# Optimization experiments

Measured on AMD Instinct MI355X. Metric: run time of the kernel, lower is better.

Reference implementation:

```python
import jax, jax.numpy as jnp
import numpy as np

B, N, D, K = 32, 196, 1024, 512  # batch, tokens (14x14), feature dim, prototypes
EPS = 1e-8  # torch F.cosine_similarity default eps


def setup_inputs() -> dict:
    key = jax.random.key(0)
    ks = jax.random.split(key, 8)
    z = jax.random.normal(ks[0], (B, N, D), jnp.float32)
    prototypes = jax.random.normal(ks[1], (K, D), jnp.float32)  # nn.Parameter(randn)
    gate_w = jax.random.normal(ks[2], (2 * D, D), jnp.float32) * 0.02  # Linear(2D->D), stored [in,out]
    gate_b = jnp.zeros((D,), jnp.float32)
    dec_w = jax.random.normal(ks[3], (D, 7 * 7 * 512), jnp.float32) * 0.02
    dec_b = jnp.zeros((7 * 7 * 512,), jnp.float32)
    ct1_w = jax.random.normal(ks[4], (512, 256, 4, 4), jnp.float32) * 0.02  # torch [in,out,kh,kw]
    ct1_b = jnp.zeros((256,), jnp.float32)
    ct2_w = jax.random.normal(ks[5], (256, 3, 4, 4), jnp.float32) * 0.02
    ct2_b = jnp.zeros((3,), jnp.float32)
    return dict(z=z, prototypes=prototypes, gate_w=gate_w, gate_b=gate_b,
                dec_w=dec_w, dec_b=dec_b, ct1_w=ct1_w, ct1_b=ct1_b,
                ct2_w=ct2_w, ct2_b=ct2_b)


def _conv_transpose(x, w, b):
    # ConvTranspose2d(k=4, stride=2, pad=1) == conv with lhs_dilation=2,
    # padding k-1-pad=2, spatially-flipped kernel, torch weight layout [in,out,kh,kw] -> IOHW.
    wf = jnp.flip(w, (2, 3))
    y = jax.lax.conv_general_dilated(
        x, wf, window_strides=(1, 1), padding=((2, 2), (2, 2)),
        lhs_dilation=(2, 2), dimension_numbers=("NCHW", "IOHW", "NCHW"))
    return y + b[None, :, None, None]


def reference(z, prototypes, gate_w, gate_b, dec_w, dec_b, ct1_w, ct1_b, ct2_w, ct2_b):
    # MemoryBank: cosine similarity of every token against every prototype
    zn = jnp.linalg.norm(z, axis=-1, keepdims=True)            # [B,N,1]
    pn = jnp.linalg.norm(prototypes, axis=-1)                  # [K]
    dots = jnp.einsum('bnd,kd->bnk', z, prototypes)            # [B,N,K]
    sim = dots / jnp.maximum(zn * pn[None, None, :], EPS)
    attn = jax.nn.softmax(sim, axis=-1)                        # [B,N,K]
    z_hat = jnp.einsum('bnk,kd->bnd', attn, prototypes)        # [B,N,D]
    # GatedFusion: sigmoid gate over concat(z, z_hat)
    gate = jax.nn.sigmoid(jnp.concatenate([z, z_hat], axis=-1) @ gate_w + gate_b)
    z_fused = gate * z + (1.0 - gate) * z_hat                  # [B,N,D]
    # Decoder (original reshape is shape-inconsistent; pool tokens -> [B,D])
    pooled = z_fused.mean(axis=1)                              # [B,D]
    h = (pooled @ dec_w + dec_b).reshape(-1, 512, 7, 7)
    h = jax.nn.relu(_conv_transpose(h, ct1_w, ct1_b))          # [B,256,14,14]
    x_recon = _conv_transpose(h, ct2_w, ct2_b)                 # [B,3,28,28]
    return x_recon, attn
```

## Files before the change

### kernel.cpp

```cpp
#include <hip/hip_runtime.h>
#include <cstdint>
#include <cstddef>
#include <cmath>

#define EPS_COS 1e-8f

typedef unsigned short u16;
typedef __attribute__((ext_vector_type(8))) short short8v;
typedef __attribute__((ext_vector_type(4))) short short4v;
typedef __attribute__((ext_vector_type(4))) float f32x4;

__device__ __forceinline__ u16 f2bf(float x) {
    unsigned int u = __float_as_uint(x);
    return (u16)((u + 0x7FFFu + ((u >> 16) & 1u)) >> 16);
}
__device__ __forceinline__ float bf2f(u16 h) {
    return __uint_as_float(((unsigned int)h) << 16);
}

__global__ __launch_bounds__(256) void norm_cvt_kernel(const float* __restrict__ src,
                                                       u16* __restrict__ dst, int dstStride,
                                                       float* __restrict__ norms) {
    int r = blockIdx.x;
    int t = threadIdx.x;
    const float4 v = *reinterpret_cast<const float4*>(&src[(size_t)r * 1024 + t * 4]);
    short4v o;
    o[0] = f2bf(v.x); o[1] = f2bf(v.y); o[2] = f2bf(v.z); o[3] = f2bf(v.w);
    *reinterpret_cast<short4v*>(&dst[(size_t)r * dstStride + t * 4]) = o;
    float ss = v.x * v.x + v.y * v.y + v.z * v.z + v.w * v.w;
#pragma unroll
    for (int off = 32; off > 0; off >>= 1) ss += __shfl_down(ss, off);
    __shared__ float red[4];
    int wave = t >> 6, lane = t & 63;
    if (lane == 0) red[wave] = ss;
    __syncthreads();
    if (t == 0) norms[r] = sqrtf(red[0] + red[1] + red[2] + red[3]);
}

__global__ __launch_bounds__(256) void transpose_cvt_kernel(const float* __restrict__ src,
                                                            u16* __restrict__ dst,
                                                            int R, int C) {
    __shared__ float tile[64][65];
    int c0 = blockIdx.x * 64, r0 = blockIdx.y * 64;
    int t = threadIdx.x;
#pragma unroll
    for (int j = 0; j < 16; ++j) {
        int idx = j * 256 + t;
        int r = idx >> 6, c = idx & 63;
        tile[r][c] = src[(size_t)(r0 + r) * C + c0 + c];
    }
    __syncthreads();
#pragma unroll
    for (int j = 0; j < 16; ++j) {
        int idx = j * 256 + t;
        int c = idx >> 6, r = idx & 63;
        dst[(size_t)(c0 + c) * R + r0 + r] = f2bf(tile[r][c]);
    }
}

__global__ __launch_bounds__(256) void prep_kernel(u16* __restrict__ hp,
                                                   const float* __restrict__ ct1w,
                                                   u16* __restrict__ wt,
                                                   const float* __restrict__ ct2w,
                                                   u16* __restrict__ wpad,
                                                   float* __restrict__ pooled) {
    int idx = blockIdx.x * 256 + threadIdx.x;
    if (idx < 165888) {
        short8v zv = {0, 0, 0, 0, 0, 0, 0, 0};
        *reinterpret_cast<short8v*>(hp + (size_t)idx * 8) = zv;
    } else if (idx < 165888 + 131072) {
        int i = idx - 165888;
        int oc = i & 255, ic = i >> 8;
        float v[16];
#pragma unroll
        for (int j = 0; j < 16; ++j) v[j] = ct1w[(size_t)i * 16 + j];
#pragma unroll
        for (int pp = 0; pp < 4; ++pp) {
            int py = pp >> 1, px = pp & 1;
#pragma unroll
            for (int tap = 0; tap < 4; ++tap) {
                int ty = tap >> 1, tx = tap & 1;
                int ky = (1 - py) + 2 * ty;
                int kx = (1 - px) + 2 * tx;
                wt[((size_t)(pp * 256 + oc)) * 2048 + ic * 4 + tap] = f2bf(v[ky * 4 + kx]);
            }
        }
    } else if (idx < 165888 + 131072 + 16384) {
        int i = idx - 165888 - 131072;
        int ic = i & 255;
        int col = i >> 8;
        float v = 0.0f;
        if (col < 48) {
            int kx = col & 3, ky = (col >> 2) & 3, oc = col >> 4;
            v = ct2w[((size_t)ic * 3 + oc) * 16 + ky * 4 + kx];
        }
        wpad[i] = f2bf(v);
    } else {
        int i = idx - 165888 - 131072 - 16384;
        *reinterpret_cast<f32x4*>(pooled + (size_t)i * 4) = (f32x4){0.f, 0.f, 0.f, 0.f};
    }
}

template <int FM, int FN, int EPI>
__global__ __launch_bounds__(256) void mfma_gemm_kernel(
    const u16* __restrict__ A, int sA, size_t zsA,
    const u16* __restrict__ B, int sB, size_t zsB,
    int M, int N, int K,
    float* __restrict__ Cf,
    u16* __restrict__ Cb, int sCb,
    const float* __restrict__ bias,
    const float* __restrict__ zf32,
    const u16* __restrict__ zhbf, int szh,
    float* __restrict__ outf) {
    constexpr int BM = FM * 32, BN = FN * 32;
    constexpr int NA = (BM * 4) / 256;
    constexpr int NB = (BN * 4) / 256;
    __shared__ __align__(16) u16 As[BM * 32];
    __shared__ __align__(16) u16 Bs[BN * 32];
    A += (size_t)blockIdx.z * zsA;
    B += (size_t)blockIdx.z * zsB;
    const int t = threadIdx.x;
    const int lane = t & 63;
    const int wid = t >> 6;
    const int wm = wid >> 1, wn = wid & 1;
    const int m0 = blockIdx.x * BM, n0 = blockIdx.y * BN;
    const int g = lane >> 4, lr = lane & 15;

    f32x4 acc[FM][FN];
#pragma unroll
    for (int i = 0; i < FM; ++i)
#pragma unroll
        for (int j = 0; j < FN; ++j) acc[i][j] = (f32x4){0.f, 0.f, 0.f, 0.f};

    short8v ra[NA], rb[NB];
#pragma unroll
    for (int j = 0; j < NA; ++j) {
        int c = j * 256 + t, row = c >> 2, ck = (c & 3) ^ ((row >> 1) & 3);
        ra[j] = *reinterpret_cast<const short8v*>(A + (size_t)(m0 + row) * sA + ck * 8);
    }
#pragma unroll
    for (int j = 0; j < NB; ++j) {
        int c = j * 256 + t, row = c >> 2, ck = (c & 3) ^ ((row >> 1) & 3);
        rb[j] = *reinterpret_cast<const short8v*>(B + (size_t)(n0 + row) * sB + ck * 8);
    }

    for (int k0 = 0; k0 < K; k0 += 32) {
        __syncthreads();
#pragma unroll
        for (int j = 0; j < NA; ++j)
            *reinterpret_cast<short8v*>(As + ((j * 256 + t) << 3)) = ra[j];
#pragma unroll
        for (int j = 0; j < NB; ++j)
            *reinterpret_cast<short8v*>(Bs + ((j * 256 + t) << 3)) = rb[j];
        __syncthreads();
        if (k0 + 32 < K) {
#pragma unroll
            for (int j = 0; j < NA; ++j) {
                int c = j * 256 + t, row = c >> 2, ck = (c & 3) ^ ((row >> 1) & 3);
                ra[j] = *reinterpret_cast<const short8v*>(A + (size_t)(m0 + row) * sA + k0 + 32 + ck * 8);
            }
#pragma unroll
            for (int j = 0; j < NB; ++j) {
                int c = j * 256 + t, row = c >> 2, ck = (c & 3) ^ ((row >> 1) & 3);
                rb[j] = *reinterpret_cast<const short8v*>(B + (size_t)(n0 + row) * sB + k0 + 32 + ck * 8);
            }
        }
        short8v af[FM], bfr[FN];
#pragma unroll
        for (int fm = 0; fm < FM; ++fm) {
            int row = wm * (FM * 16) + fm * 16 + lr;
            int ck = g ^ ((row >> 1) & 3);
            af[fm] = *reinterpret_cast<const short8v*>(As + row * 32 + ck * 8);
        }
#pragma unroll
        for (int fn = 0; fn < FN; ++fn) {
            int col = wn * (FN * 16) + fn * 16 + lr;
            int ck = g ^ ((col >> 1) & 3);
            bfr[fn] = *reinterpret_cast<const short8v*>(Bs + col * 32 + ck * 8);
        }
#pragma unroll
        for (int fm = 0; fm < FM; ++fm)
#pragma unroll
            for (int fn = 0; fn < FN; ++fn)
                acc[fm][fn] = __builtin_amdgcn_mfma_f32_16x16x32_bf16(
                    af[fm], bfr[fn], acc[fm][fn], 0, 0, 0);
    }

    if (EPI == 2) {
#pragma unroll
        for (int fn = 0; fn < FN; ++fn) {
            int col = n0 + wn * (FN * 16) + fn * 16 + lr;
            int base = m0 + wm * (FM * 16) + g * 4;
            int b0 = base / 196;
            float p0 = 0.f, p1 = 0.f;
#pragma unroll
            for (int fm = 0; fm < FM; ++fm) {
#pragma unroll
                for (int r = 0; r < 4; ++r) {
                    int row = base + fm * 16 + r;
                    float v = acc[fm][fn][r];
                    float gs = 1.0f / (1.0f + __expf(-(v + bias[col])));
                    float zv = zf32[(size_t)row * N + col];
                    float zh = bf2f(zhbf[(size_t)row * szh + col]);
                    float fused = gs * zv + (1.0f - gs) * zh;
                    bool same = (row / 196) == b0;
                    p0 += same ? fused : 0.f;
                    p1 += same ? 0.f : fused;
                }
            }
            atomicAdd(&outf[(size_t)b0 * 1024 + col], p0);
            if (p1 != 0.f) atomicAdd(&outf[(size_t)(b0 + 1) * 1024 + col], p1);
        }
    } else {
#pragma unroll
        for (int fm = 0; fm < FM; ++fm) {
#pragma unroll
            for (int fn = 0; fn < FN; ++fn) {
#pragma unroll
                for (int r = 0; r < 4; ++r) {
                    int row = m0 + wm * (FM * 16) + fm * 16 + g * 4 + r;
                    int col = n0 + wn * (FN * 16) + fn * 16 + lr;
                    float v = acc[fm][fn][r];
                    if (EPI == 0) {
                        Cf[(size_t)row * N + col] = v;
                    } else if (EPI == 1) {
                        Cb[(size_t)row * sCb + col] = f2bf(v);
                    } else {
                        if (row < 1568) {
                            float vv = fmaxf(v + bias[col], 0.0f);
                            int bb = row / 49, ss = row - bb * 49;
                            Cb[(((size_t)bb * 4 + blockIdx.z) * 49 + ss) * 256 + col] = f2bf(vv);
                        }
                    }
                }
            }
        }
    }
}

__global__ __launch_bounds__(256) void softmax_kernel(const float* __restrict__ dots,
                                                      const float* __restrict__ zn,
                                                      const float* __restrict__ pn,
                                                      float* __restrict__ attn,
                                                      u16* __restrict__ attn_bf) {
    int m = blockIdx.x;
    int t = threadIdx.x;
    float zm = zn[m];
    float d0 = dots[(size_t)m * 512 + t];
    float d1 = dots[(size_t)m * 512 + t + 256];
    float v0 = d0 / fmaxf(zm * pn[t], EPS_COS);
    float v1 = d1 / fmaxf(zm * pn[t + 256], EPS_COS);
    float mx = fmaxf(v0, v1);
#pragma unroll
    for (int off = 32; off > 0; off >>= 1) mx = fmaxf(mx, __shfl_down(mx, off));
    __shared__ float red[8];
    int wave = t >> 6, lane = t & 63;
    if (lane == 0) red[wave] = mx;
    __syncthreads();
    if (t == 0) red[4] = fmaxf(fmaxf(red[0], red[1]), fmaxf(red[2], red[3]));
    __syncthreads();
    mx = red[4];
    float e0 = expf(v0 - mx), e1 = expf(v1 - mx);
    float s = e0 + e1;
#pragma unroll
    for (int off = 32; off > 0; off >>= 1) s += __shfl_down(s, off);
    if (lane == 0) red[wave] = s;
    __syncthreads();
    if (t == 0) red[5] = 1.0f / (red[0] + red[1] + red[2] + red[3]);
    __syncthreads();
    float r = red[5];
    float a0 = e0 * r, a1 = e1 * r;
    attn[(size_t)m * 512 + t] = a0;
    attn[(size_t)m * 512 + t + 256] = a1;
    attn_bf[(size_t)m * 512 + t] = f2bf(a0);
    attn_bf[(size_t)m * 512 + t + 256] = f2bf(a1);
}

#define DEC_KC 128
__global__ __launch_bounds__(256) void dec_split_kernel(const float* __restrict__ pooled,
                                                        const float* __restrict__ dec_w,
                                                        float* __restrict__ partial) {
    const int t = threadIdx.x;
    const int lane = t & 63;
    const int wv = t >> 6;
    const int c = blockIdx.x * 256 + lane * 4;
    const int kc = blockIdx.y;
    __shared__ float pl[32][DEC_KC];
    for (int i = t; i < 32 * DEC_KC; i += 256) {
        int b = i >> 7, kk = i & (DEC_KC - 1);
        pl[b][kk] = pooled[(size_t)b * 1024 + kc * DEC_KC + kk] * (1.0f / 196.0f);
    }
    __syncthreads();
    f32x4 acc[8];
#pragma unroll
    for (int j = 0; j < 8; ++j) acc[j] = (f32x4){0.f, 0.f, 0.f, 0.f};
    const float* wp = dec_w + (size_t)(kc * DEC_KC) * 25088 + c;
#pragma unroll 8
    for (int k = 0; k < DEC_KC; ++k) {
        f32x4 w4 = *reinterpret_cast<const f32x4*>(wp + (size_t)k * 25088);
#pragma unroll
        for (int j = 0; j < 8; ++j) {
            float pv = pl[wv * 8 + j][k];
            acc[j].x = fmaf(pv, w4.x, acc[j].x);
            acc[j].y = fmaf(pv, w4.y, acc[j].y);
            acc[j].z = fmaf(pv, w4.z, acc[j].z);
            acc[j].w = fmaf(pv, w4.w, acc[j].w);
        }
    }
#pragma unroll
    for (int j = 0; j < 8; ++j) {
        int b = wv * 8 + j;
        *reinterpret_cast<f32x4*>(partial + ((size_t)kc * 32 + b) * 25088 + c) = acc[j];
    }
}

__global__ __launch_bounds__(256) void dec_reduce_kernel(const float* __restrict__ partial,
                                                         const float* __restrict__ dec_b,
                                                         u16* __restrict__ hp) {
    int c = blockIdx.x * 256 + threadIdx.x;
    int b = blockIdx.y;
    float s = dec_b[c];
#pragma unroll
    for (int kc = 0; kc < 8; ++kc)
        s += partial[((size_t)kc * 32 + b) * 25088 + c];
    int ic = c / 49, sp = c - ic * 49;
    int sy = sp / 7, sx = sp - sy * 7;
    hp[((size_t)b * 512 + ic) * 81 + (sy + 1) * 9 + sx + 1] = f2bf(s);
}

__global__ __launch_bounds__(256) void im2col_kernel(const u16* __restrict__ hp,
                                                     u16* __restrict__ A) {
    int idx = blockIdx.x * 256 + threadIdx.x;
    int k8 = idx & 255;
    int pr = idx >> 8;
    int p = pr / 1600;
    int row = pr - p * 1600;
    short8v o = {0, 0, 0, 0, 0, 0, 0, 0};
    if (row < 1568) {
        int b = row / 49, s = row - b * 49;
        int sy = s / 7, sx = s - sy * 7;
        int r0 = sy + (p >> 1) + 1;
        int c0 = sx + (p & 1) + 1;
        int ic0 = k8 * 2;
        const u16* hb = hp + ((size_t)b * 512 + ic0) * 81;
#pragma unroll
        for (int j = 0; j < 2; ++j) {
            o[j * 4 + 0] = hb[r0 * 9 + c0];
            o[j * 4 + 1] = hb[r0 * 9 + c0 - 1];
            o[j * 4 + 2] = hb[(r0 - 1) * 9 + c0];
            o[j * 4 + 3] = hb[(r0 - 1) * 9 + c0 - 1];
            hb += 81;
        }
    }
    *reinterpret_cast<short8v*>(A + (size_t)idx * 8) = o;
}

__global__ __launch_bounds__(256) void convt2_gather_kernel(const float* __restrict__ G,
                                                            const float* __restrict__ bias,
                                                            float* __restrict__ out) {
    int o = blockIdx.x * 256 + threadIdx.x;
    int ox = o % 28;
    int oy = (o / 28) % 28;
    int oc = (o / 784) % 3;
    int b = o / 2352;
    int by = (oy + 1) >> 1, bx = (ox + 1) >> 1;
    float acc = bias[oc];
#pragma unroll
    for (int ty = 0; ty < 2; ++ty) {
        int iy = by - ty;
        if ((unsigned)iy >= 14u) continue;
#pragma unroll
        for (int tx = 0; tx < 2; ++tx) {
            int ix = bx - tx;
            if ((unsigned)ix >= 14u) continue;
            int p = (iy & 1) * 2 + (ix & 1);
            int row = ((b * 4 + p) * 49) + (iy >> 1) * 7 + (ix >> 1);
            int ky = oy + 1 - 2 * iy, kx = ox + 1 - 2 * ix;
            acc += G[(size_t)row * 64 + oc * 16 + ky * 4 + kx];
        }
    }
    out[o] = acc;
}

extern "C" void kernel_launch(void* const* d_in, const int* in_sizes, int n_in,
                              void* d_out, int out_size, void* d_ws, size_t ws_size,
                              hipStream_t stream) {
    const float* z      = (const float*)d_in[0];
    const float* protos = (const float*)d_in[1];
    const float* gate_w = (const float*)d_in[2];
    const float* gate_b = (const float*)d_in[3];
    const float* dec_w  = (const float*)d_in[4];
    const float* dec_b  = (const float*)d_in[5];
    const float* ct1_w  = (const float*)d_in[6];
    const float* ct1_b  = (const float*)d_in[7];
    const float* ct2_w  = (const float*)d_in[8];
    const float* ct2_b  = (const float*)d_in[9];

    float* xout = (float*)d_out;
    float* attn = xout + 75264;

    float* w = (float*)d_ws;
    float* pn        = w;
    float* zn        = w + 512;
    float* pooled    = w + 6784;
    u16*   wt1bf     = (u16*)(w + 51840);
    u16*   protos_bf = (u16*)(w + 1100416);
    u16*   protosT   = (u16*)(w + 1362560);
    u16*   gwT       = (u16*)(w + 1624704);
    u16*   attn_bf   = (u16*)(w + 2673280);
    u16*   Abig      = (u16*)(w + 4278912);
    u16*   A_cls     = (u16*)(w + 2673280);
    float* dots      = w + 10701440;
    float* partial   = w + 10701440;
    u16*   h2cb      = (u16*)(w + 11364992);
    u16*   hp        = (u16*)(w + 17123968);
    float* G         = w + 17787520;
    u16*   wpad      = (u16*)(w + 18188928);

    prep_kernel<<<1256, 256, 0, stream>>>(hp, ct1_w, wt1bf, ct2_w, wpad, pooled);
    norm_cvt_kernel<<<6272, 256, 0, stream>>>(z, Abig, 2048, zn);
    norm_cvt_kernel<<<512, 256, 0, stream>>>(protos, protos_bf, 1024, pn);
    transpose_cvt_kernel<<<dim3(16, 8), 256, 0, stream>>>(protos, protosT, 512, 1024);
    transpose_cvt_kernel<<<dim3(16, 32), 256, 0, stream>>>(gate_w, gwT, 2048, 1024);
    mfma_gemm_kernel<2, 4, 0><<<dim3(98, 4), 256, 0, stream>>>(
        Abig, 2048, 0, protos_bf, 1024, 0, 6272, 512, 1024,
        dots, nullptr, 0, nullptr, nullptr, nullptr, 0, nullptr);
    softmax_kernel<<<6272, 256, 0, stream>>>(dots, zn, pn, attn, attn_bf);
    mfma_gemm_kernel<4, 4, 1><<<dim3(49, 8), 256, 0, stream>>>(
        attn_bf, 512, 0, protosT, 512, 0, 6272, 1024, 512,
        nullptr, Abig + 1024, 2048, nullptr, nullptr, nullptr, 0, nullptr);
    mfma_gemm_kernel<4, 4, 2><<<dim3(49, 8), 256, 0, stream>>>(
        Abig, 2048, 0, gwT, 2048, 0, 6272, 1024, 2048,
        nullptr, nullptr, 0, gate_b, z, Abig + 1024, 2048, pooled);
    dec_split_kernel<<<dim3(98, 8), 256, 0, stream>>>(pooled, dec_w, partial);
    dec_reduce_kernel<<<dim3(98, 32), 256, 0, stream>>>(partial, dec_b, hp);
    im2col_kernel<<<6400, 256, 0, stream>>>(hp, A_cls);
    mfma_gemm_kernel<2, 2, 3><<<dim3(25, 4, 4), 256, 0, stream>>>(
        A_cls, 2048, (size_t)1600 * 2048, wt1bf, 2048, (size_t)256 * 2048,
        1600, 256, 2048, nullptr, h2cb, 0, ct1_b, nullptr, nullptr, 0, nullptr);
    mfma_gemm_kernel<2, 2, 0><<<dim3(98, 1), 256, 0, stream>>>(
        h2cb, 256, 0, wpad, 256, 0, 6272, 64, 256,
        G, nullptr, 0, nullptr, nullptr, nullptr, 0, nullptr);
    convt2_gather_kernel<<<294, 256, 0, stream>>>(G, ct2_b, xout);
}
```

Measured before the change: 220.5 us.

## Widen GEMM K-tile to 64, add block swizzle, bf16 z epilogue, pipeline decoder loads

The MFMA GEMM now stages 64-wide K tiles with an XOR bank swizzle, so there are half as many barrier round-trips per K. An optional grid remap groups blocks (intended for XCD/L2 locality) and is enabled on the three large GEMMs. The gated-fusion epilogue reads z from the bf16 copy instead of fp32, which halves that traffic but adds rounding error to the pooled result. The decoder split kernel software-pipelines its weight loads four rows ahead to hide global latency.

```diff
diff --git a/kernel.cpp b/kernel.cpp
--- a/kernel.cpp
+++ b/kernel.cpp
@@ -101,7 +101,7 @@
     }
 }
 
-template <int FM, int FN, int EPI>
+template <int FM, int FN, int EPI, bool SWZ>
 __global__ __launch_bounds__(256) void mfma_gemm_kernel(
     const u16* __restrict__ A, int sA, size_t zsA,
     const u16* __restrict__ B, int sB, size_t zsB,
@@ -109,21 +109,30 @@
     float* __restrict__ Cf,
     u16* __restrict__ Cb, int sCb,
     const float* __restrict__ bias,
-    const float* __restrict__ zf32,
+    const u16* __restrict__ zbf,
     const u16* __restrict__ zhbf, int szh,
     float* __restrict__ outf) {
     constexpr int BM = FM * 32, BN = FN * 32;
-    constexpr int NA = (BM * 4) / 256;
-    constexpr int NB = (BN * 4) / 256;
-    __shared__ __align__(16) u16 As[BM * 32];
-    __shared__ __align__(16) u16 Bs[BN * 32];
+    constexpr int NA = BM / 32;
+    constexpr int NB = BN / 32;
+    __shared__ __align__(16) u16 As[BM * 64];
+    __shared__ __align__(16) u16 Bs[BN * 64];
+    int bx = blockIdx.x, by = blockIdx.y;
+    if (SWZ) {
+        int gx = gridDim.x;
+        int nwg = gx * gridDim.y;
+        int lb = by * gx + bx;
+        int flat = (lb & 7) * (nwg >> 3) + (lb >> 3);
+        bx = flat % gx;
+        by = flat / gx;
+    }
     A += (size_t)blockIdx.z * zsA;
     B += (size_t)blockIdx.z * zsB;
     const int t = threadIdx.x;
     const int lane = t & 63;
     const int wid = t >> 6;
     const int wm = wid >> 1, wn = wid & 1;
-    const int m0 = blockIdx.x * BM, n0 = blockIdx.y * BN;
+    const int m0 = bx * BM, n0 = by * BN;
     const int g = lane >> 4, lr = lane & 15;
 
     f32x4 acc[FM][FN];
@@ -135,55 +144,62 @@
     short8v ra[NA], rb[NB];
 #pragma unroll
     for (int j = 0; j < NA; ++j) {
-        int c = j * 256 + t, row = c >> 2, ck = (c & 3) ^ ((row >> 1) & 3);
+        int c = j * 256 + t, row = c >> 3, ck = c & 7;
         ra[j] = *reinterpret_cast<const short8v*>(A + (size_t)(m0 + row) * sA + ck * 8);
     }
 #pragma unroll
     for (int j = 0; j < NB; ++j) {
-        int c = j * 256 + t, row = c >> 2, ck = (c & 3) ^ ((row >> 1) & 3);
+        int c = j * 256 + t, row = c >> 3, ck = c & 7;
         rb[j] = *reinterpret_cast<const short8v*>(B + (size_t)(n0 + row) * sB + ck * 8);
     }
 
-    for (int k0 = 0; k0 < K; k0 += 32) {
+    for (int k0 = 0; k0 < K; k0 += 64) {
         __syncthreads();
 #pragma unroll
-        for (int j = 0; j < NA; ++j)
-            *reinterpret_cast<short8v*>(As + ((j * 256 + t) << 3)) = ra[j];
-#pragma unroll
-        for (int j = 0; j < NB; ++j)
-            *reinterpret_cast<short8v*>(Bs + ((j * 256 + t) << 3)) = rb[j];
+        for (int j = 0; j < NA; ++j) {
+            int c = j * 256 + t, row = c >> 3, ck = c & 7;
+            *reinterpret_cast<short8v*>(As + row * 64 + ((ck ^ (row & 7)) << 3)) = ra[j];
+        }
+#pragma unroll
+        for (int j = 0; j < NB; ++j) {
+            int c = j * 256 + t, row = c >> 3, ck = c & 7;
+            *reinterpret_cast<short8v*>(Bs + row * 64 + ((ck ^ (row & 7)) << 3)) = rb[j];
+        }
         __syncthreads();
-        if (k0 + 32 < K) {
+        if (k0 + 64 < K) {
 #pragma unroll
             for (int j = 0; j < NA; ++j) {
-                int c = j * 256 + t, row = c >> 2, ck = (c & 3) ^ ((row >> 1) & 3);
-                ra[j] = *reinterpret_cast<const short8v*>(A + (size_t)(m0 + row) * sA + k0 + 32 + ck * 8);
+                int c = j * 256 + t, row = c >> 3, ck = c & 7;
+                ra[j] = *reinterpret_cast<const short8v*>(A + (size_t)(m0 + row) * sA + k0 + 64 + ck * 8);
             }
 #pragma unroll
             for (int j = 0; j < NB; ++j) {
-                int c = j * 256 + t, row = c >> 2, ck = (c & 3) ^ ((row >> 1) & 3);
-                rb[j] = *reinterpret_cast<const short8v*>(B + (size_t)(n0 + row) * sB + k0 + 32 + ck * 8);
-            }
-        }
-        short8v af[FM], bfr[FN];
-#pragma unroll
-        for (int fm = 0; fm < FM; ++fm) {
-            int row = wm * (FM * 16) + fm * 16 + lr;
-            int ck = g ^ ((row >> 1) & 3);
-            af[fm] = *reinterpret_cast<const short8v*>(As + row * 32 + ck * 8);
-        }
-#pragma unroll
-        for (int fn = 0; fn < FN; ++fn) {
-            int col = wn * (FN * 16) + fn * 16 + lr;
-            int ck = g ^ ((col >> 1) & 3);
-            bfr[fn] = *reinterpret_cast<const short8v*>(Bs + col * 32 + ck * 8);
-        }
-#pragma unroll
-        for (int fm = 0; fm < FM; ++fm)
-#pragma unroll
-            for (int fn = 0; fn < FN; ++fn)
-                acc[fm][fn] = __builtin_amdgcn_mfma_f32_16x16x32_bf16(
-                    af[fm], bfr[fn], acc[fm][fn], 0, 0, 0);
+                int c = j * 256 + t, row = c >> 3, ck = c & 7;
+                rb[j] = *reinterpret_cast<const short8v*>(B + (size_t)(n0 + row) * sB + k0 + 64 + ck * 8);
+            }
+        }
+#pragma unroll
+        for (int kk = 0; kk < 2; ++kk) {
+            short8v af[FM], bfr[FN];
+#pragma unroll
+            for (int fm = 0; fm < FM; ++fm) {
+                int row = wm * (FM * 16) + fm * 16 + lr;
+                int rc = (kk * 4 + g) ^ (row & 7);
+                af[fm] = *reinterpret_cast<const short8v*>(As + row * 64 + rc * 8);
+            }
+#pragma unroll
+            for (int fn = 0; fn < FN; ++fn) {
+                int col = wn * (FN * 16) + fn * 16 + lr;
+                int rc = (kk * 4 + g) ^ (col & 7);
+                bfr[fn] = *reinterpret_cast<const short8v*>(Bs + col * 64 + rc * 8);
+            }
+#pragma unroll
+            for (int fm = 0; fm < FM; ++fm)
+#pragma unroll
+                for (int fn = 0; fn < FN; ++fn)
+                    acc[fm][fn] = __builtin_amdgcn_mfma_f32_16x16x32_bf16(
+                        af[fm], bfr[fn], acc[fm][fn], 0, 0, 0);
+        }
     }
 
     if (EPI == 2) {
@@ -200,7 +216,7 @@
                     int row = base + fm * 16 + r;
                     float v = acc[fm][fn][r];
                     float gs = 1.0f / (1.0f + __expf(-(v + bias[col])));
-                    float zv = zf32[(size_t)row * N + col];
+                    float zv = bf2f(zbf[(size_t)row * szh + col]);
                     float zh = bf2f(zhbf[(size_t)row * szh + col]);
                     float fused = gs * zv + (1.0f - gs) * zh;
                     bool same = (row / 196) == b0;
@@ -295,18 +311,34 @@
 #pragma unroll
     for (int j = 0; j < 8; ++j) acc[j] = (f32x4){0.f, 0.f, 0.f, 0.f};
     const float* wp = dec_w + (size_t)(kc * DEC_KC) * 25088 + c;
-#pragma unroll 8
-    for (int k = 0; k < DEC_KC; ++k) {
-        f32x4 w4 = *reinterpret_cast<const f32x4*>(wp + (size_t)k * 25088);
-#pragma unroll
-        for (int j = 0; j < 8; ++j) {
-            float pv = pl[wv * 8 + j][k];
-            acc[j].x = fmaf(pv, w4.x, acc[j].x);
-            acc[j].y = fmaf(pv, w4.y, acc[j].y);
-            acc[j].z = fmaf(pv, w4.z, acc[j].z);
-            acc[j].w = fmaf(pv, w4.w, acc[j].w);
-        }
-    }
+
+#define LDW(kk) (*reinterpret_cast<const f32x4*>(wp + (size_t)(kk) * 25088))
+#define FMA4(wreg, kk)                                          \
+    _Pragma("unroll") for (int j = 0; j < 8; ++j) {             \
+        float pv = pl[wv * 8 + j][kk];                          \
+        acc[j].x = fmaf(pv, wreg.x, acc[j].x);                  \
+        acc[j].y = fmaf(pv, wreg.y, acc[j].y);                  \
+        acc[j].z = fmaf(pv, wreg.z, acc[j].z);                  \
+        acc[j].w = fmaf(pv, wreg.w, acc[j].w);                  \
+    }
+
+    f32x4 w0 = LDW(0), w1 = LDW(1), w2 = LDW(2), w3 = LDW(3);
+#pragma unroll 1
+    for (int k = 0; k < DEC_KC; k += 4) {
+        int kn = (k + 4) & (DEC_KC - 1);
+        f32x4 n0 = LDW(kn + 0);
+        f32x4 n1 = LDW(kn + 1);
+        f32x4 n2 = LDW(kn + 2);
+        f32x4 n3 = LDW(kn + 3);
+        FMA4(w0, k + 0);
+        FMA4(w1, k + 1);
+        FMA4(w2, k + 2);
+        FMA4(w3, k + 3);
+        w0 = n0; w1 = n1; w2 = n2; w3 = n3;
+    }
+#undef LDW
+#undef FMA4
+
 #pragma unroll
     for (int j = 0; j < 8; ++j) {
         int b = wv * 8 + j;
@@ -422,23 +454,23 @@
     norm_cvt_kernel<<<512, 256, 0, stream>>>(protos, protos_bf, 1024, pn);
     transpose_cvt_kernel<<<dim3(16, 8), 256, 0, stream>>>(protos, protosT, 512, 1024);
     transpose_cvt_kernel<<<dim3(16, 32), 256, 0, stream>>>(gate_w, gwT, 2048, 1024);
-    mfma_gemm_kernel<2, 4, 0><<<dim3(98, 4), 256, 0, stream>>>(
+    mfma_gemm_kernel<2, 4, 0, true><<<dim3(98, 4), 256, 0, stream>>>(
         Abig, 2048, 0, protos_bf, 1024, 0, 6272, 512, 1024,
         dots, nullptr, 0, nullptr, nullptr, nullptr, 0, nullptr);
     softmax_kernel<<<6272, 256, 0, stream>>>(dots, zn, pn, attn, attn_bf);
-    mfma_gemm_kernel<4, 4, 1><<<dim3(49, 8), 256, 0, stream>>>(
+    mfma_gemm_kernel<4, 4, 1, true><<<dim3(49, 8), 256, 0, stream>>>(
         attn_bf, 512, 0, protosT, 512, 0, 6272, 1024, 512,
         nullptr, Abig + 1024, 2048, nullptr, nullptr, nullptr, 0, nullptr);
-    mfma_gemm_kernel<4, 4, 2><<<dim3(49, 8), 256, 0, stream>>>(
+    mfma_gemm_kernel<4, 4, 2, true><<<dim3(49, 8), 256, 0, stream>>>(
         Abig, 2048, 0, gwT, 2048, 0, 6272, 1024, 2048,
-        nullptr, nullptr, 0, gate_b, z, Abig + 1024, 2048, pooled);
+        nullptr, nullptr, 0, gate_b, Abig, Abig + 1024, 2048, pooled);
     dec_split_kernel<<<dim3(98, 8), 256, 0, stream>>>(pooled, dec_w, partial);
     dec_reduce_kernel<<<dim3(98, 32), 256, 0, stream>>>(partial, dec_b, hp);
     im2col_kernel<<<6400, 256, 0, stream>>>(hp, A_cls);
-    mfma_gemm_kernel<2, 2, 3><<<dim3(25, 4, 4), 256, 0, stream>>>(
+    mfma_gemm_kernel<2, 2, 3, false><<<dim3(25, 4, 4), 256, 0, stream>>>(
         A_cls, 2048, (size_t)1600 * 2048, wt1bf, 2048, (size_t)256 * 2048,
         1600, 256, 2048, nullptr, h2cb, 0, ct1_b, nullptr, nullptr, 0, nullptr);
-    mfma_gemm_kernel<2, 2, 0><<<dim3(98, 1), 256, 0, stream>>>(
+    mfma_gemm_kernel<2, 2, 0, false><<<dim3(98, 1), 256, 0, stream>>>(
         h2cb, 256, 0, wpad, 256, 0, 6272, 64, 256,
         G, nullptr, 0, nullptr, nullptr, nullptr, 0, nullptr);
     convt2_gather_kernel<<<294, 256, 0, stream>>>(G, ct2_b, xout);
```

After: 216.3 us. Within noise of the previous version (-1.9%).
